# Kernel optimization log

Measured on AMD Instinct MI355X. Metric: run time of the kernel, lower is better.

## Reference

```python
import jax, jax.numpy as jnp
import numpy as np

TOPK = 2
ALPHA_AUX = 0.02

def setup_inputs() -> dict:
    key = jax.random.key(0)
    ks = jax.random.split(key, 6)
    B, T, D, E, H = 2, 2048, 1024, 16, 1536
    s_in = 1.0 / np.sqrt(D)
    s_h = 1.0 / np.sqrt(H)
    return {
        "x": jax.random.normal(ks[0], (B, T, D), dtype=jnp.float32),
        "router_w": jax.random.normal(ks[1], (E, D), dtype=jnp.float32) * s_in,
        "w1": jax.random.normal(ks[2], (E, H, D), dtype=jnp.float32) * s_in,
        "b1": jax.random.normal(ks[3], (E, H), dtype=jnp.float32) * 0.01,
        "w2": jax.random.normal(ks[4], (E, D, H), dtype=jnp.float32) * s_h,
        "b2": jax.random.normal(ks[5], (E, D), dtype=jnp.float32) * 0.01,
    }

def reference(x, router_w, w1, b1, w2, b2):
    B, T, D = x.shape
    E = router_w.shape[0]
    N = B * T
    x_flat = x.reshape(N, D)

    # Router: top-k logits -> softmax gates -> dense dispatch matrix [N, E]
    logits = x_flat @ router_w.T                      # [N, E]
    vals, idx = jax.lax.top_k(logits, TOPK)           # [N, K]
    gate = jax.nn.softmax(vals, axis=-1)              # [N, K]
    rows = jnp.arange(N)[:, None]
    dispatch = jnp.zeros((N, E), dtype=x.dtype).at[rows, idx].set(gate)

    # Expert MLPs computed densely over all experts; gate==0 masks unselected,
    # reproducing the gather-MLP-scatter math exactly.
    h = jnp.einsum('nd,ehd->neh', x_flat, w1) + b1    # [N, E, H]
    h = jax.nn.gelu(h, approximate=True)              # tanh GELU
    y = jnp.einsum('neh,edh->ned', h, w2) + b2        # [N, E, D]
    out = jnp.einsum('ne,ned->nd', dispatch, y).reshape(B, T, D)

    # Auxiliary load-balancing loss
    tok_per_expert = (dispatch > 0).sum(0).astype(jnp.float32)  # [E]
    f_i = tok_per_expert / tok_per_expert.sum()
    m_i = dispatch.sum(0) / jnp.clip(tok_per_expert, 1.0, None)
    aux_loss = ALPHA_AUX * (f_i * m_i).mean()
    return out, aux_loss
```

## Files before the change

kernel.cpp:

```cpp
#include <hip/hip_runtime.h>
#include <hip/hip_bf16.h>
#include <math.h>

#define N_TOK 4096
#define DIM   1024
#define NEXP  16
#define HID   1536
#define TOPK2 2
#define NASSIGN (N_TOK * TOPK2)

#define MAX_ITEMS 80
#define G1_BLOCKS (MAX_ITEMS * 12)
#define G2_BLOCKS (MAX_ITEMS * 8)

typedef __attribute__((ext_vector_type(8))) short short8;
typedef __attribute__((ext_vector_type(4))) float floatx4;
typedef unsigned short u16;

#define GLOAD_LDS16(gp, lp)                                                     \
    __builtin_amdgcn_global_load_lds(                                           \
        (const __attribute__((address_space(1))) unsigned int*)(gp),            \
        (__attribute__((address_space(3))) unsigned int*)(lp), 16, 0, 0)

__device__ __forceinline__ u16 bf16u(float f) {
    __hip_bfloat16 h = __float2bfloat16(f);
    return *(u16*)&h;
}

__device__ __forceinline__ short8 cvt8(float4 a, float4 b) {
    short8 r;
    r[0] = (short)bf16u(a.x); r[1] = (short)bf16u(a.y);
    r[2] = (short)bf16u(a.z); r[3] = (short)bf16u(a.w);
    r[4] = (short)bf16u(b.x); r[5] = (short)bf16u(b.y);
    r[6] = (short)bf16u(b.z); r[7] = (short)bf16u(b.w);
    return r;
}

__global__ __launch_bounds__(256)
void router_kernel(const float* __restrict__ x, const float* __restrict__ rw,
                   int* __restrict__ idx, float* __restrict__ gate,
                   u16* __restrict__ x_bf) {
    int tid = threadIdx.x;
    int tb = blockIdx.x * 16;
    __shared__ float xs[16][68];
    __shared__ float rs[16][68];
    __shared__ float lg[16][17];

    int t = tid >> 4, e = tid & 15;
    int srow = tid >> 4, scol = (tid & 15) * 4;

    float acc = 0.f;
    for (int k0 = 0; k0 < DIM; k0 += 64) {
        float4 xv = *(const float4*)&x[(size_t)(tb + srow) * DIM + k0 + scol];
        *(float4*)&xs[srow][scol] = xv;
        *(float4*)&rs[srow][scol] = *(const float4*)&rw[(size_t)srow * DIM + k0 + scol];
        {
            ushort4 o;
            o.x = bf16u(xv.x); o.y = bf16u(xv.y); o.z = bf16u(xv.z); o.w = bf16u(xv.w);
            *(ushort4*)&x_bf[(size_t)(tb + srow) * DIM + k0 + scol] = o;
        }
        __syncthreads();
        const float2* xp = (const float2*)xs[t];
        const float2* rp = (const float2*)rs[e];
        #pragma unroll
        for (int k = 0; k < 32; k++) {
            float2 a = xp[k], b = rp[k];
            acc = fmaf(a.x, b.x, acc);
            acc = fmaf(a.y, b.y, acc);
        }
        __syncthreads();
    }
    lg[t][e] = acc;
    __syncthreads();

    if (tid < 16) {
        int n = tb + tid;
        float v0 = -3.402823466e+38f, v1 = -3.402823466e+38f;
        int i0 = 0, i1 = 0;
        #pragma unroll
        for (int ee = 0; ee < NEXP; ee++) {
            float v = lg[tid][ee];
            if (v > v0) { v1 = v0; i1 = i0; v0 = v; i0 = ee; }
            else if (v > v1) { v1 = v; i1 = ee; }
        }
        float e1 = expf(v1 - v0);
        float inv = 1.f / (1.f + e1);
        idx[2 * n] = i0; idx[2 * n + 1] = i1;
        gate[2 * n] = inv; gate[2 * n + 1] = e1 * inv;
    }
}

__global__ __launch_bounds__(256)
void plan_kernel(const int* __restrict__ idx, const float* __restrict__ gate,
                 int* __restrict__ offsets, int* __restrict__ tlist,
                 int* __restrict__ slot_of,
                 int* __restrict__ wl, int* __restrict__ wcount,
                 float* __restrict__ aux_out) {
    __shared__ int cnt_s[16];
    __shared__ float gs_s[16];
    __shared__ int pos_s[16];
    __shared__ int offs_s[17];
    int tid = threadIdx.x;
    if (tid < 16) { cnt_s[tid] = 0; gs_s[tid] = 0.f; pos_s[tid] = 0; }
    __syncthreads();
    for (int i = tid; i < NASSIGN; i += 256) {
        int e = idx[i];
        atomicAdd(&cnt_s[e], 1);
        atomicAdd(&gs_s[e], gate[i]);
    }
    __syncthreads();
    if (tid == 0) {
        int acc = 0;
        for (int e = 0; e < NEXP; e++) { offs_s[e] = acc; acc += cnt_s[e]; }
        offs_s[NEXP] = acc;
        float tot = (float)acc;
        float s = 0.f;
        for (int e = 0; e < NEXP; e++) {
            float c = (float)cnt_s[e];
            s += (c / tot) * (gs_s[e] / fmaxf(c, 1.f));
        }
        *aux_out = 0.02f * (s / (float)NEXP);
        int m = 0;
        for (int e = 0; e < NEXP; e++) {
            int nt = (cnt_s[e] + 127) >> 7;
            for (int rt = 0; rt < nt; rt++) wl[m++] = (e << 8) | rt;
        }
        *wcount = m;
    }
    __syncthreads();
    if (tid < 17) offsets[tid] = offs_s[tid];
    for (int i = tid; i < NASSIGN; i += 256) {
        int e = idx[i];
        int p = atomicAdd(&pos_s[e], 1);
        int s = offs_s[e] + p;
        tlist[s] = i;
        slot_of[i] = s;
    }
}

__device__ __forceinline__ float gelu_tanh(float v) {
    float v3 = v * v * v;
    float t = tanhf(0.7978845608028654f * (v + 0.044715f * v3));
    return 0.5f * v * (1.f + t);
}


__global__ __launch_bounds__(256)
void gemm1_kernel(const u16* __restrict__ xb, const float* __restrict__ w1,
                  const float* __restrict__ b1,
                  const int* __restrict__ offsets, const int* __restrict__ tlist,
                  const int* __restrict__ wl, const int* __restrict__ wcount,
                  u16* __restrict__ h_bf) {
    int bid = blockIdx.x;
    int item = bid / 12;
    if (item >= *wcount) return;
    int colt = bid - item * 12;
    int w = wl[item];
    int e = w >> 8, rt = w & 255;
    int beg = offsets[e], ne = offsets[e + 1] - beg;
    int row0 = rt * 128, col0 = colt * 128;

    __shared__ u16 As[2][128 * 32];
    __shared__ u16 Bs[2][128 * 32];

    int tid = threadIdx.x;
    int wave = tid >> 6, lane = tid & 63;
    int wm = wave & 1, wn = wave >> 1;

    int koff = (((lane & 3) ^ ((lane >> 3) & 3)) * 8);
    const u16* aptr[2];
    #pragma unroll
    for (int q = 0; q < 2; q++) {
        int lrow = wave * 32 + q * 16 + (lane >> 2);
        int gi = beg + row0 + lrow;
        int gi2 = (row0 + lrow < ne) ? gi : beg;
        int tok = tlist[gi2] >> 1;
        aptr[q] = xb + (size_t)tok * DIM + koff;
    }

    int brow = tid >> 1;
    int bh   = tid & 1;
    const float* bsrc = w1 + (size_t)(e * HID + col0 + brow) * DIM + bh * 16;
    int sz = (brow >> 1) & 3;
    int bc0 = (2 * bh) ^ sz;
    int bc1 = (2 * bh + 1) ^ sz;

    int rchunk = (((lane >> 4) ^ ((lane >> 1) & 3)) * 8);

    floatx4 acc[4][4] = {};
    float4 f0, f1, f2, f3;

    auto STAGE_A = [&](int kt, int b) {
        #pragma unroll
        for (int q = 0; q < 2; q++)
            GLOAD_LDS16(aptr[q] + kt * 32, &As[b][(wave * 32 + q * 16) * 32]);
    };
    auto LOAD_B = [&](int kt) {
        const float4* p = (const float4*)(bsrc + kt * 32);
        f0 = p[0]; f1 = p[1]; f2 = p[2]; f3 = p[3];
    };
    auto WRITE_B = [&](int b) {
        *(short8*)&Bs[b][brow * 32 + bc0 * 8] = cvt8(f0, f1);
        *(short8*)&Bs[b][brow * 32 + bc1 * 8] = cvt8(f2, f3);
    };
    auto CONSUME = [&](int b) {
        short8 af[4], bf_[4];
        #pragma unroll
        for (int mi = 0; mi < 4; mi++)
            af[mi] = *(const short8*)&As[b][(wm * 64 + mi * 16 + (lane & 15)) * 32 + rchunk];
        #pragma unroll
        for (int nj = 0; nj < 4; nj++)
            bf_[nj] = *(const short8*)&Bs[b][(wn * 64 + nj * 16 + (lane & 15)) * 32 + rchunk];
        #pragma unroll
        for (int mi = 0; mi < 4; mi++)
            #pragma unroll
            for (int nj = 0; nj < 4; nj++)
                acc[mi][nj] = __builtin_amdgcn_mfma_f32_16x16x32_bf16(af[mi], bf_[nj], acc[mi][nj], 0, 0, 0);
    };

    const int NT = DIM / 32;
    LOAD_B(0); STAGE_A(0, 0); WRITE_B(0);
    __syncthreads();
    int cur = 0;
    for (int t = 0; t < NT - 1; ++t) {
        LOAD_B(t + 1);
        STAGE_A(t + 1, cur ^ 1);
        CONSUME(cur);
        WRITE_B(cur ^ 1);
        __syncthreads();
        cur ^= 1;
    }
    CONSUME(cur);

    #pragma unroll
    for (int mi = 0; mi < 4; mi++) {
        #pragma unroll
        for (int r = 0; r < 4; r++) {
            int lrow = wm * 64 + mi * 16 + (lane >> 4) * 4 + r;
            if (row0 + lrow >= ne) continue;
            size_t orow = (size_t)(beg + row0 + lrow);
            #pragma unroll
            for (int nj = 0; nj < 4; nj++) {
                int col = col0 + wn * 64 + nj * 16 + (lane & 15);
                float v = acc[mi][nj][r] + b1[e * HID + col];
                h_bf[orow * HID + col] = bf16u(gelu_tanh(v));
            }
        }
    }
}

__global__ __launch_bounds__(256)
void gemm2_kernel(const u16* __restrict__ h_bf, const float* __restrict__ w2,
                  const float* __restrict__ b2,
                  const int* __restrict__ offsets, const int* __restrict__ tlist,
                  const int* __restrict__ wl, const int* __restrict__ wcount,
                  const float* __restrict__ gate, float* __restrict__ y) {
    int bid = blockIdx.x;
    int item = bid >> 3;
    if (item >= *wcount) return;
    int colt = bid & 7;
    int w = wl[item];
    int e = w >> 8, rt = w & 255;
    int beg = offsets[e], ne = offsets[e + 1] - beg;
    int row0 = rt * 128, col0 = colt * 128;

    __shared__ u16 As[2][128 * 32];
    __shared__ u16 Bs[2][128 * 32];

    int tid = threadIdx.x;
    int wave = tid >> 6, lane = tid & 63;
    int wm = wave & 1, wn = wave >> 1;

    int koff = (((lane & 3) ^ ((lane >> 3) & 3)) * 8);
    const u16* aptr[2];
    #pragma unroll
    for (int q = 0; q < 2; q++) {
        int lrow = wave * 32 + q * 16 + (lane >> 2);
        int gi = beg + row0 + lrow;
        int gi2 = (row0 + lrow < ne) ? gi : beg;
        aptr[q] = h_bf + (size_t)gi2 * HID + koff;
    }

    int brow = tid >> 1;
    int bh   = tid & 1;
    const float* bsrc = w2 + (size_t)(e * DIM + col0 + brow) * HID + bh * 16;
    int sz = (brow >> 1) & 3;
    int bc0 = (2 * bh) ^ sz;
    int bc1 = (2 * bh + 1) ^ sz;

    int rchunk = (((lane >> 4) ^ ((lane >> 1) & 3)) * 8);

    floatx4 acc[4][4] = {};
    float4 f0, f1, f2, f3;

    auto STAGE_A = [&](int kt, int b) {
        #pragma unroll
        for (int q = 0; q < 2; q++)
            GLOAD_LDS16(aptr[q] + kt * 32, &As[b][(wave * 32 + q * 16) * 32]);
    };
    auto LOAD_B = [&](int kt) {
        const float4* p = (const float4*)(bsrc + kt * 32);
        f0 = p[0]; f1 = p[1]; f2 = p[2]; f3 = p[3];
    };
    auto WRITE_B = [&](int b) {
        *(short8*)&Bs[b][brow * 32 + bc0 * 8] = cvt8(f0, f1);
        *(short8*)&Bs[b][brow * 32 + bc1 * 8] = cvt8(f2, f3);
    };
    auto CONSUME = [&](int b) {
        short8 af[4], bf_[4];
        #pragma unroll
        for (int mi = 0; mi < 4; mi++)
            af[mi] = *(const short8*)&As[b][(wm * 64 + mi * 16 + (lane & 15)) * 32 + rchunk];
        #pragma unroll
        for (int nj = 0; nj < 4; nj++)
            bf_[nj] = *(const short8*)&Bs[b][(wn * 64 + nj * 16 + (lane & 15)) * 32 + rchunk];
        #pragma unroll
        for (int mi = 0; mi < 4; mi++)
            #pragma unroll
            for (int nj = 0; nj < 4; nj++)
                acc[mi][nj] = __builtin_amdgcn_mfma_f32_16x16x32_bf16(af[mi], bf_[nj], acc[mi][nj], 0, 0, 0);
    };

    const int NT = HID / 32;
    LOAD_B(0); STAGE_A(0, 0); WRITE_B(0);
    __syncthreads();
    int cur = 0;
    for (int t = 0; t < NT - 1; ++t) {
        LOAD_B(t + 1);
        STAGE_A(t + 1, cur ^ 1);
        CONSUME(cur);
        WRITE_B(cur ^ 1);
        __syncthreads();
        cur ^= 1;
    }
    CONSUME(cur);

    #pragma unroll
    for (int mi = 0; mi < 4; mi++) {
        #pragma unroll
        for (int r = 0; r < 4; r++) {
            int lrow = wm * 64 + mi * 16 + (lane >> 4) * 4 + r;
            if (row0 + lrow >= ne) continue;
            int slot = beg + row0 + lrow;
            int t = tlist[slot];
            float g = gate[t];
            #pragma unroll
            for (int nj = 0; nj < 4; nj++) {
                int col = col0 + wn * 64 + nj * 16 + (lane & 15);
                float v = g * (acc[mi][nj][r] + b2[e * DIM + col]);
                y[(size_t)slot * DIM + col] = v;
            }
        }
    }
}

__global__ __launch_bounds__(256)
void combine_kernel(const float* __restrict__ y, const int* __restrict__ slot_of,
                    float* __restrict__ out) {
    int t = blockIdx.x;
    int c4 = threadIdx.x;
    int s0 = slot_of[2 * t], s1 = slot_of[2 * t + 1];
    float4 a = ((const float4*)(y + (size_t)s0 * DIM))[c4];
    float4 b = ((const float4*)(y + (size_t)s1 * DIM))[c4];
    float4 o;
    o.x = a.x + b.x; o.y = a.y + b.y; o.z = a.z + b.z; o.w = a.w + b.w;
    ((float4*)(out + (size_t)t * DIM))[c4] = o;
}

extern "C" void kernel_launch(void* const* d_in, const int* in_sizes, int n_in,
                              void* d_out, int out_size, void* d_ws, size_t ws_size,
                              hipStream_t stream) {
    const float* x  = (const float*)d_in[0];
    const float* rw = (const float*)d_in[1];
    const float* w1 = (const float*)d_in[2];
    const float* b1 = (const float*)d_in[3];
    const float* w2 = (const float*)d_in[4];
    const float* b2 = (const float*)d_in[5];
    float* out = (float*)d_out;

    char* ws = (char*)d_ws;
    int*   offsets = (int*)(ws + 192);
    int*   wcount  = (int*)(ws + 384);
    int*   wl      = (int*)(ws + 512);
    int*   idx     = (int*)(ws + 4096);
    float* gate    = (float*)(ws + 4096 + 4 * NASSIGN);
    int*   tlist   = (int*)(ws + 4096 + 8 * NASSIGN);
    int*   slot_of = (int*)(ws + 4096 + 12 * NASSIGN);
    u16*   x_bf    = (u16*)(ws + (256 << 10));
    u16*   h_bf    = x_bf + (size_t)N_TOK * DIM;
    float* y       = (float*)(h_bf + (size_t)NASSIGN * HID);

    router_kernel<<<N_TOK / 16, 256, 0, stream>>>(x, rw, idx, gate, x_bf);
    plan_kernel<<<1, 256, 0, stream>>>(idx, gate, offsets, tlist, slot_of,
                                       wl, wcount, out + (size_t)N_TOK * DIM);
    gemm1_kernel<<<G1_BLOCKS, 256, 0, stream>>>(
        x_bf, w1, b1, offsets, tlist, wl, wcount, h_bf);
    gemm2_kernel<<<G2_BLOCKS, 256, 0, stream>>>(
        h_bf, w2, b2, offsets, tlist, wl, wcount, gate, y);
    combine_kernel<<<N_TOK, 256, 0, stream>>>(y, slot_of, out);
}
```

Measured before the change: 456.7 us.

## Pre-convert expert weights to bf16 and stream both GEMM operands directly into LDS

Adds a conversion pass, folded into the router launch as extra blocks, that turns w1 and w2 into bf16 copies in the workspace. Both expert GEMMs then load the weight tile with direct global-to-LDS loads, dropping the per-tile fp32 register load, conversion and LDS write. The row tile shrinks from 128 to 64 tokens, with the plan and MAX_ITEMS adjusted, to give more blocks and less padding. The cost is a full read and write of the weights on every call, and the output buffer y now aliases the bf16 w1 copy.

```diff
diff --git a/kernel.cpp b/kernel.cpp
--- a/kernel.cpp
+++ b/kernel.cpp
@@ -9,9 +9,11 @@
 #define TOPK2 2
 #define NASSIGN (N_TOK * TOPK2)
 
-#define MAX_ITEMS 80
+#define MAX_ITEMS 144
 #define G1_BLOCKS (MAX_ITEMS * 12)
 #define G2_BLOCKS (MAX_ITEMS * 8)
+#define W_ELEMS   (NEXP * HID * DIM)
+#define CVT_BLOCKS (W_ELEMS / 4 / 256)
 
 typedef __attribute__((ext_vector_type(8))) short short8;
 typedef __attribute__((ext_vector_type(4))) float floatx4;
@@ -27,20 +29,27 @@
     return *(u16*)&h;
 }
 
-__device__ __forceinline__ short8 cvt8(float4 a, float4 b) {
-    short8 r;
-    r[0] = (short)bf16u(a.x); r[1] = (short)bf16u(a.y);
-    r[2] = (short)bf16u(a.z); r[3] = (short)bf16u(a.w);
-    r[4] = (short)bf16u(b.x); r[5] = (short)bf16u(b.y);
-    r[6] = (short)bf16u(b.z); r[7] = (short)bf16u(b.w);
-    return r;
-}
-
-__global__ __launch_bounds__(256)
-void router_kernel(const float* __restrict__ x, const float* __restrict__ rw,
-                   int* __restrict__ idx, float* __restrict__ gate,
-                   u16* __restrict__ x_bf) {
+__device__ __forceinline__ void cvt_one4(const float* __restrict__ src,
+                                         u16* __restrict__ dst, int i) {
+    float4 v = ((const float4*)src)[i];
+    ushort4 o;
+    o.x = bf16u(v.x); o.y = bf16u(v.y); o.z = bf16u(v.z); o.w = bf16u(v.w);
+    ((ushort4*)dst)[i] = o;
+}
+
+__global__ __launch_bounds__(256)
+void router_cvtw_kernel(const float* __restrict__ x, const float* __restrict__ rw,
+                        int* __restrict__ idx, float* __restrict__ gate,
+                        u16* __restrict__ x_bf,
+                        const float* __restrict__ w1src, u16* __restrict__ w1dst,
+                        const float* __restrict__ w2src, u16* __restrict__ w2dst) {
     int tid = threadIdx.x;
+    if (blockIdx.x >= 256) {
+        int c = blockIdx.x - 256;
+        if (c < CVT_BLOCKS) cvt_one4(w1src, w1dst, c * 256 + tid);
+        else                cvt_one4(w2src, w2dst, (c - CVT_BLOCKS) * 256 + tid);
+        return;
+    }
     int tb = blockIdx.x * 16;
     __shared__ float xs[16][68];
     __shared__ float rs[16][68];
@@ -122,7 +131,7 @@
         *aux_out = 0.02f * (s / (float)NEXP);
         int m = 0;
         for (int e = 0; e < NEXP; e++) {
-            int nt = (cnt_s[e] + 127) >> 7;
+            int nt = (cnt_s[e] + 63) >> 6;
             for (int rt = 0; rt < nt; rt++) wl[m++] = (e << 8) | rt;
         }
         *wcount = m;
@@ -146,7 +155,7 @@
 
 
 __global__ __launch_bounds__(256)
-void gemm1_kernel(const u16* __restrict__ xb, const float* __restrict__ w1,
+void gemm1_kernel(const u16* __restrict__ xb, const u16* __restrict__ w1b,
                   const float* __restrict__ b1,
                   const int* __restrict__ offsets, const int* __restrict__ tlist,
                   const int* __restrict__ wl, const int* __restrict__ wcount,
@@ -158,9 +167,9 @@
     int w = wl[item];
     int e = w >> 8, rt = w & 255;
     int beg = offsets[e], ne = offsets[e + 1] - beg;
-    int row0 = rt * 128, col0 = colt * 128;
-
-    __shared__ u16 As[2][128 * 32];
+    int row0 = rt * 64, col0 = colt * 128;
+
+    __shared__ u16 As[2][64 * 32];
     __shared__ u16 Bs[2][128 * 32];
 
     int tid = threadIdx.x;
@@ -168,75 +177,58 @@
     int wm = wave & 1, wn = wave >> 1;
 
     int koff = (((lane & 3) ^ ((lane >> 3) & 3)) * 8);
-    const u16* aptr[2];
+    int lrowA = wave * 16 + (lane >> 2);
+    int giA = (row0 + lrowA < ne) ? (beg + row0 + lrowA) : beg;
+    const u16* aptr = xb + (size_t)(tlist[giA] >> 1) * DIM + koff;
+    const u16* bptr[2];
     #pragma unroll
     for (int q = 0; q < 2; q++) {
-        int lrow = wave * 32 + q * 16 + (lane >> 2);
-        int gi = beg + row0 + lrow;
-        int gi2 = (row0 + lrow < ne) ? gi : beg;
-        int tok = tlist[gi2] >> 1;
-        aptr[q] = xb + (size_t)tok * DIM + koff;
-    }
-
-    int brow = tid >> 1;
-    int bh   = tid & 1;
-    const float* bsrc = w1 + (size_t)(e * HID + col0 + brow) * DIM + bh * 16;
-    int sz = (brow >> 1) & 3;
-    int bc0 = (2 * bh) ^ sz;
-    int bc1 = (2 * bh + 1) ^ sz;
+        int lrowB = wave * 32 + q * 16 + (lane >> 2);
+        int n = col0 + lrowB;
+        bptr[q] = w1b + (size_t)(e * HID + n) * DIM + koff;
+    }
 
     int rchunk = (((lane >> 4) ^ ((lane >> 1) & 3)) * 8);
 
-    floatx4 acc[4][4] = {};
-    float4 f0, f1, f2, f3;
-
-    auto STAGE_A = [&](int kt, int b) {
+    floatx4 acc[2][4] = {};
+
+    auto STAGE = [&](int kt, int b) {
+        GLOAD_LDS16(aptr + kt * 32, &As[b][(wave * 16) * 32]);
         #pragma unroll
         for (int q = 0; q < 2; q++)
-            GLOAD_LDS16(aptr[q] + kt * 32, &As[b][(wave * 32 + q * 16) * 32]);
-    };
-    auto LOAD_B = [&](int kt) {
-        const float4* p = (const float4*)(bsrc + kt * 32);
-        f0 = p[0]; f1 = p[1]; f2 = p[2]; f3 = p[3];
-    };
-    auto WRITE_B = [&](int b) {
-        *(short8*)&Bs[b][brow * 32 + bc0 * 8] = cvt8(f0, f1);
-        *(short8*)&Bs[b][brow * 32 + bc1 * 8] = cvt8(f2, f3);
+            GLOAD_LDS16(bptr[q] + kt * 32, &Bs[b][(wave * 32 + q * 16) * 32]);
     };
     auto CONSUME = [&](int b) {
-        short8 af[4], bf_[4];
-        #pragma unroll
-        for (int mi = 0; mi < 4; mi++)
-            af[mi] = *(const short8*)&As[b][(wm * 64 + mi * 16 + (lane & 15)) * 32 + rchunk];
+        short8 af[2], bf_[4];
+        #pragma unroll
+        for (int mi = 0; mi < 2; mi++)
+            af[mi] = *(const short8*)&As[b][(wm * 32 + mi * 16 + (lane & 15)) * 32 + rchunk];
         #pragma unroll
         for (int nj = 0; nj < 4; nj++)
             bf_[nj] = *(const short8*)&Bs[b][(wn * 64 + nj * 16 + (lane & 15)) * 32 + rchunk];
         #pragma unroll
-        for (int mi = 0; mi < 4; mi++)
+        for (int mi = 0; mi < 2; mi++)
             #pragma unroll
             for (int nj = 0; nj < 4; nj++)
                 acc[mi][nj] = __builtin_amdgcn_mfma_f32_16x16x32_bf16(af[mi], bf_[nj], acc[mi][nj], 0, 0, 0);
     };
 
     const int NT = DIM / 32;
-    LOAD_B(0); STAGE_A(0, 0); WRITE_B(0);
+    STAGE(0, 0);
     __syncthreads();
     int cur = 0;
-    for (int t = 0; t < NT - 1; ++t) {
-        LOAD_B(t + 1);
-        STAGE_A(t + 1, cur ^ 1);
+    for (int t = 0; t < NT; ++t) {
+        if (t + 1 < NT) STAGE(t + 1, cur ^ 1);
         CONSUME(cur);
-        WRITE_B(cur ^ 1);
         __syncthreads();
         cur ^= 1;
     }
-    CONSUME(cur);
 
     #pragma unroll
-    for (int mi = 0; mi < 4; mi++) {
+    for (int mi = 0; mi < 2; mi++) {
         #pragma unroll
         for (int r = 0; r < 4; r++) {
-            int lrow = wm * 64 + mi * 16 + (lane >> 4) * 4 + r;
+            int lrow = wm * 32 + mi * 16 + (lane >> 4) * 4 + r;
             if (row0 + lrow >= ne) continue;
             size_t orow = (size_t)(beg + row0 + lrow);
             #pragma unroll
@@ -250,7 +242,7 @@
 }
 
 __global__ __launch_bounds__(256)
-void gemm2_kernel(const u16* __restrict__ h_bf, const float* __restrict__ w2,
+void gemm2_kernel(const u16* __restrict__ h_bf, const u16* __restrict__ w2b,
                   const float* __restrict__ b2,
                   const int* __restrict__ offsets, const int* __restrict__ tlist,
                   const int* __restrict__ wl, const int* __restrict__ wcount,
@@ -262,9 +254,9 @@
     int w = wl[item];
     int e = w >> 8, rt = w & 255;
     int beg = offsets[e], ne = offsets[e + 1] - beg;
-    int row0 = rt * 128, col0 = colt * 128;
-
-    __shared__ u16 As[2][128 * 32];
+    int row0 = rt * 64, col0 = colt * 128;
+
+    __shared__ u16 As[2][64 * 32];
     __shared__ u16 Bs[2][128 * 32];
 
     int tid = threadIdx.x;
@@ -272,74 +264,58 @@
     int wm = wave & 1, wn = wave >> 1;
 
     int koff = (((lane & 3) ^ ((lane >> 3) & 3)) * 8);
-    const u16* aptr[2];
+    int lrowA = wave * 16 + (lane >> 2);
+    int giA = (row0 + lrowA < ne) ? (beg + row0 + lrowA) : beg;
+    const u16* aptr = h_bf + (size_t)giA * HID + koff;
+    const u16* bptr[2];
     #pragma unroll
     for (int q = 0; q < 2; q++) {
-        int lrow = wave * 32 + q * 16 + (lane >> 2);
-        int gi = beg + row0 + lrow;
-        int gi2 = (row0 + lrow < ne) ? gi : beg;
-        aptr[q] = h_bf + (size_t)gi2 * HID + koff;
-    }
-
-    int brow = tid >> 1;
-    int bh   = tid & 1;
-    const float* bsrc = w2 + (size_t)(e * DIM + col0 + brow) * HID + bh * 16;
-    int sz = (brow >> 1) & 3;
-    int bc0 = (2 * bh) ^ sz;
-    int bc1 = (2 * bh + 1) ^ sz;
+        int lrowB = wave * 32 + q * 16 + (lane >> 2);
+        int n = col0 + lrowB;
+        bptr[q] = w2b + (size_t)(e * DIM + n) * HID + koff;
+    }
 
     int rchunk = (((lane >> 4) ^ ((lane >> 1) & 3)) * 8);
 
-    floatx4 acc[4][4] = {};
-    float4 f0, f1, f2, f3;
-
-    auto STAGE_A = [&](int kt, int b) {
+    floatx4 acc[2][4] = {};
+
+    auto STAGE = [&](int kt, int b) {
+        GLOAD_LDS16(aptr + kt * 32, &As[b][(wave * 16) * 32]);
         #pragma unroll
         for (int q = 0; q < 2; q++)
-            GLOAD_LDS16(aptr[q] + kt * 32, &As[b][(wave * 32 + q * 16) * 32]);
-    };
-    auto LOAD_B = [&](int kt) {
-        const float4* p = (const float4*)(bsrc + kt * 32);
-        f0 = p[0]; f1 = p[1]; f2 = p[2]; f3 = p[3];
-    };
-    auto WRITE_B = [&](int b) {
-        *(short8*)&Bs[b][brow * 32 + bc0 * 8] = cvt8(f0, f1);
-        *(short8*)&Bs[b][brow * 32 + bc1 * 8] = cvt8(f2, f3);
+            GLOAD_LDS16(bptr[q] + kt * 32, &Bs[b][(wave * 32 + q * 16) * 32]);
     };
     auto CONSUME = [&](int b) {
-        short8 af[4], bf_[4];
-        #pragma unroll
-        for (int mi = 0; mi < 4; mi++)
-            af[mi] = *(const short8*)&As[b][(wm * 64 + mi * 16 + (lane & 15)) * 32 + rchunk];
+        short8 af[2], bf_[4];
+        #pragma unroll
+        for (int mi = 0; mi < 2; mi++)
+            af[mi] = *(const short8*)&As[b][(wm * 32 + mi * 16 + (lane & 15)) * 32 + rchunk];
         #pragma unroll
         for (int nj = 0; nj < 4; nj++)
             bf_[nj] = *(const short8*)&Bs[b][(wn * 64 + nj * 16 + (lane & 15)) * 32 + rchunk];
         #pragma unroll
-        for (int mi = 0; mi < 4; mi++)
+        for (int mi = 0; mi < 2; mi++)
             #pragma unroll
             for (int nj = 0; nj < 4; nj++)
                 acc[mi][nj] = __builtin_amdgcn_mfma_f32_16x16x32_bf16(af[mi], bf_[nj], acc[mi][nj], 0, 0, 0);
     };
 
     const int NT = HID / 32;
-    LOAD_B(0); STAGE_A(0, 0); WRITE_B(0);
+    STAGE(0, 0);
     __syncthreads();
     int cur = 0;
-    for (int t = 0; t < NT - 1; ++t) {
-        LOAD_B(t + 1);
-        STAGE_A(t + 1, cur ^ 1);
+    for (int t = 0; t < NT; ++t) {
+        if (t + 1 < NT) STAGE(t + 1, cur ^ 1);
         CONSUME(cur);
-        WRITE_B(cur ^ 1);
         __syncthreads();
         cur ^= 1;
     }
-    CONSUME(cur);
 
     #pragma unroll
-    for (int mi = 0; mi < 4; mi++) {
+    for (int mi = 0; mi < 2; mi++) {
         #pragma unroll
         for (int r = 0; r < 4; r++) {
-            int lrow = wm * 64 + mi * 16 + (lane >> 4) * 4 + r;
+            int lrow = wm * 32 + mi * 16 + (lane >> 4) * 4 + r;
             if (row0 + lrow >= ne) continue;
             int slot = beg + row0 + lrow;
             int t = tlist[slot];
@@ -388,14 +364,17 @@
     int*   slot_of = (int*)(ws + 4096 + 12 * NASSIGN);
     u16*   x_bf    = (u16*)(ws + (256 << 10));
     u16*   h_bf    = x_bf + (size_t)N_TOK * DIM;
-    float* y       = (float*)(h_bf + (size_t)NASSIGN * HID);
-
-    router_kernel<<<N_TOK / 16, 256, 0, stream>>>(x, rw, idx, gate, x_bf);
+    u16*   w1_bf   = h_bf + (size_t)NASSIGN * HID;
+    u16*   w2_bf   = w1_bf + (size_t)W_ELEMS;
+    float* y       = (float*)w1_bf;
+
+    router_cvtw_kernel<<<256 + 2 * CVT_BLOCKS, 256, 0, stream>>>(
+        x, rw, idx, gate, x_bf, w1, w1_bf, w2, w2_bf);
     plan_kernel<<<1, 256, 0, stream>>>(idx, gate, offsets, tlist, slot_of,
                                        wl, wcount, out + (size_t)N_TOK * DIM);
     gemm1_kernel<<<G1_BLOCKS, 256, 0, stream>>>(
-        x_bf, w1, b1, offsets, tlist, wl, wcount, h_bf);
+        x_bf, w1_bf, b1, offsets, tlist, wl, wcount, h_bf);
     gemm2_kernel<<<G2_BLOCKS, 256, 0, stream>>>(
-        h_bf, w2, b2, offsets, tlist, wl, wcount, gate, y);
+        h_bf, w2_bf, b2, offsets, tlist, wl, wcount, gate, y);
     combine_kernel<<<N_TOK, 256, 0, stream>>>(y, slot_of, out);
 }
```

After: 419.3 us. 8.2% less time.
